# Performance work log

Measured on AMD Instinct MI355X. Metric: run time of the kernel, lower is better.

The kernel has to match this reference:

```python
import jax, jax.numpy as jnp
import numpy as np
from jax import lax

K = 13  # sizearea
DN = ('NCHW', 'OIHW', 'NCHW')


def conv(x, W, b):
    y = lax.conv_general_dilated(x, W, (1, 1), 'SAME', dimension_numbers=DN)
    return y + b[None, :, None, None]


def setup_inputs() -> dict:
    key = jax.random.key(0)
    ks = jax.random.split(key, 4)
    x = jax.random.normal(ks[0], (8, 1, 256, 256), dtype=jnp.float32)
    W1 = jax.random.normal(ks[1], (64, 1, 3, 3), dtype=jnp.float32) * 0.1
    b1 = jnp.zeros((64,), dtype=jnp.float32)
    W2 = jax.random.normal(ks[2], (64, 64, 3, 3), dtype=jnp.float32) * 0.05
    b2 = jnp.zeros((64,), dtype=jnp.float32)
    W3 = jax.random.normal(ks[3], (K * K, 64, 3, 3), dtype=jnp.float32) * 0.05
    b3 = jnp.zeros((K * K,), dtype=jnp.float32)
    return {'x': x, 'W1': W1, 'b1': b1, 'W2': W2, 'b2': b2, 'W3': W3, 'b3': b3}


def reference(x, W1, b1, W2, b2, W3, b3):
    # weight-predicting CNN (sar_data=False -> x used directly)
    h = jax.nn.relu(conv(x, W1, b1))
    h = jax.nn.relu(conv(h, W2, b2))
    w = conv(h, W3, b3)                       # (B, K*K, H, W)

    B, C, H, Wd = x.shape                     # C == 1
    # w.permute(0,2,3,1).view(B,1,H,W,K,K)
    wr = jnp.transpose(w, (0, 2, 3, 1)).reshape(B, 1, H, Wd, K, K)

    Ho, Wo = H - K + 1, Wd - K + 1            # unfold with stride 1, no pad
    pr, pc = (H - Ho) // 2, (Wd - Wo) // 2    # center-crop of weight maps
    wc = wr[:, :, pr:H - pr, pc:Wd - pc]      # (B,1,Ho,Wo,K,K)

    # patches[b,0,i,j,u,v] = x[b,0,i+u,j+v]  (C=1, so channel-major flatten is just (kh,kw))
    patches = lax.conv_general_dilated_patches(
        x, (K, K), (1, 1), 'VALID', dimension_numbers=DN)   # (B, K*K, Ho, Wo)
    patches = patches.reshape(B, 1, K, K, Ho, Wo).transpose(0, 1, 4, 5, 2, 3)

    # per-pixel weighted sum over the KxK window
    y = jnp.einsum('bchwuv,bchwuv->bchw', patches, wc)       # (B,1,Ho,Wo)
    return y
```

## Files before the change

kernel.cpp:

```cpp
#include <hip/hip_runtime.h>

#define HW 256
#define BATCH 8
#define C 64
#define HO 244
#define NPAD 192
#define KTOT 576

typedef __bf16 bf16x8 __attribute__((ext_vector_type(8)));
typedef float f32x16 __attribute__((ext_vector_type(16)));
typedef float f32x2 __attribute__((ext_vector_type(2)));
typedef unsigned short us8 __attribute__((ext_vector_type(8)));

__device__ inline unsigned short fbf(float f) {
    return __builtin_bit_cast(unsigned short, (__bf16)f);
}

__device__ inline float bf2f(unsigned short s) {
    union { unsigned int u; float f; } c;
    c.u = ((unsigned int)s) << 16;
    return c.f;
}

__global__ __launch_bounds__(256) void repack_w_kernel(
    const float* __restrict__ W2, const float* __restrict__ W3,
    unsigned short* __restrict__ B2g, unsigned short* __restrict__ B3g)
{
    int idx = blockIdx.x * 256 + threadIdx.x;
    if (idx < 36 * 2 * C * 8) {
        int e = idx & 7;
        int r = idx >> 3;
        int n = r & 63;
        int s = r >> 6;
        int khalf = s & 1;
        int kstep = s >> 1;
        int chunk = kstep >> 2, ks = kstep & 3;
        int ci = ks * 16 + khalf * 8 + e;
        B2g[idx] = fbf(W2[((size_t)n * C + ci) * 9 + chunk]);
    } else {
        int j = idx - 36 * 2 * C * 8;
        if (j >= 36 * 2 * NPAD * 8) return;
        int e = j & 7;
        int r = j >> 3;
        int n = r % NPAD;
        int s = r / NPAD;
        int khalf = s & 1;
        int kstep = s >> 1;
        int chunk = kstep >> 2, ks = kstep & 3;
        int ci = ks * 16 + khalf * 8 + e;
        float v = (n < 169) ? W3[((size_t)n * C + ci) * 9 + chunk] : 0.f;
        B3g[j] = fbf(v);
    }
}

__global__ __launch_bounds__(256, 3) void conv2_fused_kernel(
    const float* __restrict__ x, const float* __restrict__ W1,
    const float* __restrict__ b1, const unsigned short* __restrict__ W2r,
    const float* __restrict__ b2, unsigned short* __restrict__ h2)
{
    __shared__ unsigned short Ash[396 * 66];
    __shared__ unsigned short Xsh[8 * 68];

    const int t = threadIdx.x;
    const int lane = t & 63;
    const int wave = t >> 6;
    const int b  = blockIdx.z;
    const int h0 = blockIdx.y * 4;
    const int w0 = blockIdx.x * 64;

    const int col   = lane & 31;
    const int khalf = lane >> 5;
    const int mrow_base = wave * 64;

    const float* __restrict__ xplane = x + ((size_t)b << 16);
#pragma unroll
    for (int it = 0; it < 3; ++it) {
        int li = it * 256 + t;
        if (li < 8 * 68) {
            int rr = li / 68, cc = li - rr * 68;
            int hh = h0 - 2 + rr, ww = w0 - 2 + cc;
            bool ok = (hh >= 0) && (hh < HW) && (ww >= 0) && (ww < HW);
            Xsh[li] = ok ? fbf(xplane[hh * HW + ww]) : (unsigned short)0;
        }
    }

    const int g4 = t & 15;
    f32x2 w01[9], w23[9];
    f32x2 bia01, bia23;
    bia01[0] = b1[g4 * 4 + 0]; bia01[1] = b1[g4 * 4 + 1];
    bia23[0] = b1[g4 * 4 + 2]; bia23[1] = b1[g4 * 4 + 3];
#pragma unroll
    for (int q = 0; q < 9; ++q) {
        w01[q][0] = W1[(g4 * 4 + 0) * 9 + q];
        w01[q][1] = W1[(g4 * 4 + 1) * 9 + q];
        w23[q][0] = W1[(g4 * 4 + 2) * 9 + q];
        w23[q][1] = W1[(g4 * 4 + 3) * 9 + q];
    }

    __syncthreads();

    for (int it = 0; it < 25; ++it) {
        int li = it * 256 + t;
        if (li < 6336) {
            int p = li >> 4;
            int pr = p / 66, pc = p - pr * 66;
            int hh = h0 - 1 + pr, ww = w0 - 1 + pc;
            unsigned short ov[4];
            if (hh >= 0 && hh < HW && ww >= 0 && ww < HW) {
                const unsigned short* xb = Xsh + pr * 68 + pc;
                f32x2 a01 = bia01, a23 = bia23;
#pragma unroll
                for (int i = 0; i < 3; ++i)
#pragma unroll
                    for (int j = 0; j < 3; ++j) {
                        float xv = bf2f(xb[i * 68 + j]);
                        f32x2 xv2; xv2[0] = xv; xv2[1] = xv;
                        a01 += xv2 * w01[i * 3 + j];
                        a23 += xv2 * w23[i * 3 + j];
                    }
                ov[0] = fbf(fmaxf(a01[0], 0.f));
                ov[1] = fbf(fmaxf(a01[1], 0.f));
                ov[2] = fbf(fmaxf(a23[0], 0.f));
                ov[3] = fbf(fmaxf(a23[1], 0.f));
            } else {
#pragma unroll
                for (int u = 0; u < 4; ++u) ov[u] = 0;
            }
            *(uint2*)(Ash + p * 66 + g4 * 4) = *(uint2*)ov;
        }
    }

    const unsigned short* bbase = W2r + ((size_t)khalf * C + col) * 8;
    us8 bcur0 = *(const us8*)(bbase);
    us8 bcur1 = *(const us8*)(bbase + 32 * 8);
    us8 bnx0  = *(const us8*)(bbase + (size_t)(2 * C * 8));
    us8 bnx1  = *(const us8*)(bbase + (size_t)(2 * C * 8) + 32 * 8);

    f32x16 acc[2][2];
#pragma unroll
    for (int ai = 0; ai < 2; ++ai)
#pragma unroll
        for (int nb = 0; nb < 2; ++nb)
#pragma unroll
            for (int r = 0; r < 16; ++r) acc[ai][nb][r] = 0.f;

    __syncthreads();

#pragma unroll
    for (int kstep = 0; kstep < 36; ++kstep) {
        const int chunk = kstep >> 2, ks = kstep & 3;
        const int ii = chunk / 3, jj = chunk - ii * 3;
        const int pixbase = (wave + ii) * 66 + jj;
        us8 bn0, bn1;
        if (kstep + 2 < 36) {
            const unsigned short* bp = bbase + (size_t)(kstep + 2) * (2 * C * 8);
            bn0 = *(const us8*)(bp);
            bn1 = *(const us8*)(bp + 32 * 8);
        }
        const int koff = ks * 16 + khalf * 8;
        bf16x8 a0 = __builtin_bit_cast(bf16x8, *(const us8*)(Ash + (pixbase + col) * 66 + koff));
        bf16x8 a1 = __builtin_bit_cast(bf16x8, *(const us8*)(Ash + (pixbase + col + 32) * 66 + koff));
        bf16x8 v0 = __builtin_bit_cast(bf16x8, bcur0);
        bf16x8 v1 = __builtin_bit_cast(bf16x8, bcur1);
        acc[0][0] = __builtin_amdgcn_mfma_f32_32x32x16_bf16(a0, v0, acc[0][0], 0, 0, 0);
        acc[0][1] = __builtin_amdgcn_mfma_f32_32x32x16_bf16(a0, v1, acc[0][1], 0, 0, 0);
        acc[1][0] = __builtin_amdgcn_mfma_f32_32x32x16_bf16(a1, v0, acc[1][0], 0, 0, 0);
        acc[1][1] = __builtin_amdgcn_mfma_f32_32x32x16_bf16(a1, v1, acc[1][1], 0, 0, 0);
        bcur0 = bnx0; bcur1 = bnx1;
        bnx0 = bn0; bnx1 = bn1;
    }

#pragma unroll
    for (int nb = 0; nb < 2; ++nb) {
        const int n = nb * 32 + col;
        const float bias = b2[n];
#pragma unroll
        for (int ai = 0; ai < 2; ++ai) {
#pragma unroll
            for (int r = 0; r < 16; ++r) {
                int m = mrow_base + ai * 32 + (r & 3) + ((r >> 2) << 3) + (khalf << 2);
                int h = h0 + (m >> 6), w = w0 + (m & 63);
                float val = fmaxf(acc[ai][nb][r] + bias, 0.f);
                h2[(((size_t)b * HW + h) * HW + w) * C + n] = fbf(val);
            }
        }
    }
}

__global__ __launch_bounds__(512, 3) void conv3_mfma_kernel(
    const float* __restrict__ x, const unsigned short* __restrict__ h2,
    const unsigned short* __restrict__ Bg, const float* __restrict__ b3,
    float* __restrict__ y)
{
    __shared__ unsigned short Ash[396 * 72];
    __shared__ float Xsh[16 * 77];
    __shared__ float red[8][64];

    const int t = threadIdx.x;
    const int lane = t & 63;
    const int wave = t >> 6;
    const int b   = blockIdx.z;
    const int ho0 = blockIdx.y * 4;
    const int wo0 = blockIdx.x * 64;

    const int col   = lane & 31;
    const int khalf = lane >> 5;
    const int rsel      = wave >> 1;
    const int mrow_base = rsel * 64;
    const int nbase     = (wave & 1) * 96;

    f32x16 acc[2][3];
#pragma unroll
    for (int mi = 0; mi < 2; ++mi)
#pragma unroll
        for (int ni = 0; ni < 3; ++ni)
#pragma unroll
            for (int r = 0; r < 16; ++r) acc[mi][ni][r] = 0.f;

#pragma unroll
    for (int it = 0; it < 7; ++it) {
        int li = it * 512 + t;
        if (li < 396 * 8) {
            int p = li >> 3, g = li & 7;
            int row = p / 66, cl = p - row * 66;
            int ww = wo0 + 5 + cl; ww = ww < 255 ? ww : 255;
            size_t src = (((size_t)b * HW + (ho0 + 5 + row)) * HW + ww) * C + g * 8;
            *(uint4*)(Ash + p * 72 + g * 8) = *(const uint4*)(h2 + src);
        }
    }
    {
        const float* __restrict__ xplane = x + ((size_t)b << 16);
#pragma unroll
        for (int it = 0; it < 3; ++it) {
            int li = it * 512 + t;
            if (li < 16 * 76) {
                int rr = li / 76, cc = li - rr * 76;
                int ww = wo0 + cc; ww = ww < 255 ? ww : 255;
                Xsh[rr * 77 + cc] = xplane[(ho0 + rr) * HW + ww];
            }
        }
    }

    const unsigned short* bbase = Bg + ((size_t)khalf * NPAD + nbase + col) * 8;
    us8 bcur0 = *(const us8*)(bbase);
    us8 bcur1 = *(const us8*)(bbase + 32 * 8);
    us8 bcur2 = *(const us8*)(bbase + 64 * 8);
    us8 bnx0  = *(const us8*)(bbase + (size_t)(2 * NPAD * 8));
    us8 bnx1  = *(const us8*)(bbase + (size_t)(2 * NPAD * 8) + 32 * 8);
    us8 bnx2  = *(const us8*)(bbase + (size_t)(2 * NPAD * 8) + 64 * 8);

    __syncthreads();

#pragma unroll
    for (int kstep = 0; kstep < 36; ++kstep) {
        const int chunk = kstep >> 2, ks = kstep & 3;
        const int ii = chunk / 3, jj = chunk - ii * 3;
        const int pixbase = (rsel + ii) * 66 + jj;
        us8 bn0, bn1, bn2;
        if (kstep + 2 < 36) {
            const unsigned short* bp = bbase + (size_t)(kstep + 2) * (2 * NPAD * 8);
            bn0 = *(const us8*)(bp);
            bn1 = *(const us8*)(bp + 32 * 8);
            bn2 = *(const us8*)(bp + 64 * 8);
        }
        const int koff = ks * 16 + khalf * 8;
        bf16x8 a0 = __builtin_bit_cast(bf16x8, *(const us8*)(Ash + (pixbase + col) * 72 + koff));
        bf16x8 a1 = __builtin_bit_cast(bf16x8, *(const us8*)(Ash + (pixbase + col + 32) * 72 + koff));
        bf16x8 v0 = __builtin_bit_cast(bf16x8, bcur0);
        bf16x8 v1 = __builtin_bit_cast(bf16x8, bcur1);
        bf16x8 v2 = __builtin_bit_cast(bf16x8, bcur2);
        acc[0][0] = __builtin_amdgcn_mfma_f32_32x32x16_bf16(a0, v0, acc[0][0], 0, 0, 0);
        acc[0][1] = __builtin_amdgcn_mfma_f32_32x32x16_bf16(a0, v1, acc[0][1], 0, 0, 0);
        acc[0][2] = __builtin_amdgcn_mfma_f32_32x32x16_bf16(a0, v2, acc[0][2], 0, 0, 0);
        acc[1][0] = __builtin_amdgcn_mfma_f32_32x32x16_bf16(a1, v0, acc[1][0], 0, 0, 0);
        acc[1][1] = __builtin_amdgcn_mfma_f32_32x32x16_bf16(a1, v1, acc[1][1], 0, 0, 0);
        acc[1][2] = __builtin_amdgcn_mfma_f32_32x32x16_bf16(a1, v2, acc[1][2], 0, 0, 0);
        bcur0 = bnx0; bcur1 = bnx1; bcur2 = bnx2;
        bnx0 = bn0; bnx1 = bn1; bnx2 = bn2;
    }

    int   qv[3], uo[3], vo[3];
    float b3v[3];
#pragma unroll
    for (int ni = 0; ni < 3; ++ni) {
        int q = nbase + ni * 32 + col;
        qv[ni] = q;
        int u = q / 13;
        uo[ni] = u;
        vo[ni] = q - u * 13;
        b3v[ni] = (q < 169) ? b3[q] : 0.f;
    }

    float partial[2][16];
#pragma unroll
    for (int mi = 0; mi < 2; ++mi)
#pragma unroll
        for (int r = 0; r < 16; ++r) {
            int mrow = mi * 32 + (r & 3) + ((r >> 2) << 3) + (khalf << 2);
            bool wok = (wo0 + mrow) < HO;
            float p = 0.f;
#pragma unroll
            for (int ni = 0; ni < 3; ++ni) {
                if (qv[ni] < 169 && wok) {
                    float s = acc[mi][ni][r] + b3v[ni];
                    p += s * Xsh[(rsel + uo[ni]) * 77 + mrow + vo[ni]];
                }
            }
            partial[mi][r] = p;
        }

#pragma unroll
    for (int mi = 0; mi < 2; ++mi)
#pragma unroll
        for (int r = 0; r < 16; ++r) {
            float p = partial[mi][r];
#pragma unroll
            for (int d = 1; d < 32; d <<= 1) p += __shfl_xor(p, d, 64);
            partial[mi][r] = p;
        }

    if (col == 0) {
#pragma unroll
        for (int mi = 0; mi < 2; ++mi)
#pragma unroll
            for (int r = 0; r < 16; ++r) {
                int mrow = mi * 32 + (r & 3) + ((r >> 2) << 3) + (khalf << 2);
                red[wave][mrow] = partial[mi][r];
            }
    }
    __syncthreads();

    if (t < 256) {
        int row_sel = t >> 6, m = t & 63;
        float val = red[row_sel * 2][m] + red[row_sel * 2 + 1][m];
        int wo = wo0 + m, ho = ho0 + row_sel;
        if (wo < HO)
            y[((size_t)b * HO + ho) * HO + wo] = val;
    }
}

extern "C" void kernel_launch(void* const* d_in, const int* in_sizes, int n_in,
                              void* d_out, int out_size, void* d_ws, size_t ws_size,
                              hipStream_t stream) {
    const float* x  = (const float*)d_in[0];
    const float* W1 = (const float*)d_in[1];
    const float* b1 = (const float*)d_in[2];
    const float* W2 = (const float*)d_in[3];
    const float* b2 = (const float*)d_in[4];
    const float* W3 = (const float*)d_in[5];
    const float* b3 = (const float*)d_in[6];
    float* out = (float*)d_out;

    unsigned short* h2  = (unsigned short*)d_ws;
    unsigned short* W2r = h2 + (size_t)BATCH * HW * HW * C;
    unsigned short* W3r = W2r + (size_t)36 * 2 * C * 8;

    repack_w_kernel<<<576, 256, 0, stream>>>(W2, W3, W2r, W3r);
    conv2_fused_kernel<<<dim3(4, 64, 8), 256, 0, stream>>>(x, W1, b1, W2r, b2, h2);
    conv3_mfma_kernel<<<dim3(4, 61, 8), 512, 0, stream>>>(x, h2, W3r, b3, out);
}
```

Measured before the change: 240.3 us.

## Register-block conv1 per thread, add MFMA priority, use DPP reductions in epilogue

The first-layer conv in the conv2 kernel now computes six adjacent output pixels per thread from vectorized row loads. This reuses input values across the sliding window and cuts the loop from 25 iterations to 5. The MFMA block in the conv2 k-loop is wrapped in s_setprio to favour matrix issue. The conv3 epilogue loads x values as float4 and replaces the 5-step shfl_xor reduction with DPP row operations. The DPP lane pattern and the choice of col==16 as the writer carry correctness risk, and the larger per-thread accumulator set raises register pressure.

```diff
diff --git a/kernel.cpp b/kernel.cpp
--- a/kernel.cpp
+++ b/kernel.cpp
@@ -9,6 +9,7 @@
 
 typedef __bf16 bf16x8 __attribute__((ext_vector_type(8)));
 typedef float f32x16 __attribute__((ext_vector_type(16)));
+typedef float f32x4 __attribute__((ext_vector_type(4)));
 typedef float f32x2 __attribute__((ext_vector_type(2)));
 typedef unsigned short us8 __attribute__((ext_vector_type(8)));
 
@@ -20,6 +21,13 @@
     union { unsigned int u; float f; } c;
     c.u = ((unsigned int)s) << 16;
     return c.f;
+}
+
+template <int CTRL>
+__device__ inline float dpp_add(float v) {
+    int s = __builtin_bit_cast(int, v);
+    int m = __builtin_amdgcn_update_dpp(s, s, CTRL, 0xF, 0xF, true);
+    return v + __builtin_bit_cast(float, m);
 }
 
 __global__ __launch_bounds__(256) void repack_w_kernel(
@@ -99,34 +107,52 @@
 
     __syncthreads();
 
-    for (int it = 0; it < 25; ++it) {
+#pragma unroll
+    for (int it = 0; it < 5; ++it) {
         int li = it * 256 + t;
-        if (li < 6336) {
-            int p = li >> 4;
-            int pr = p / 66, pc = p - pr * 66;
-            int hh = h0 - 1 + pr, ww = w0 - 1 + pc;
-            unsigned short ov[4];
-            if (hh >= 0 && hh < HW && ww >= 0 && ww < HW) {
-                const unsigned short* xb = Xsh + pr * 68 + pc;
-                f32x2 a01 = bia01, a23 = bia23;
-#pragma unroll
-                for (int i = 0; i < 3; ++i)
+        if (li < 1056) {
+            int w = li >> 4;
+            int pr = w / 11;
+            int pc0 = (w - pr * 11) * 6;
+            int hh = h0 - 1 + pr;
+            bool okrow = (hh >= 0) && (hh < HW);
+            const unsigned short* xb = Xsh + pr * 68 + pc0;
+
+            f32x2 ac01[6], ac23[6];
+#pragma unroll
+            for (int k2 = 0; k2 < 6; ++k2) { ac01[k2] = bia01; ac23[k2] = bia23; }
+
+#pragma unroll
+            for (int i = 0; i < 3; ++i) {
+                us8 xw = *(const us8*)(xb + i * 68);
+                float xr[8];
+#pragma unroll
+                for (int e = 0; e < 8; ++e) xr[e] = bf2f(xw[e]);
+#pragma unroll
+                for (int k2 = 0; k2 < 6; ++k2)
 #pragma unroll
                     for (int j = 0; j < 3; ++j) {
-                        float xv = bf2f(xb[i * 68 + j]);
-                        f32x2 xv2; xv2[0] = xv; xv2[1] = xv;
-                        a01 += xv2 * w01[i * 3 + j];
-                        a23 += xv2 * w23[i * 3 + j];
+                        f32x2 xv2; xv2[0] = xr[k2 + j]; xv2[1] = xr[k2 + j];
+                        ac01[k2] += xv2 * w01[i * 3 + j];
+                        ac23[k2] += xv2 * w23[i * 3 + j];
                     }
-                ov[0] = fbf(fmaxf(a01[0], 0.f));
-                ov[1] = fbf(fmaxf(a01[1], 0.f));
-                ov[2] = fbf(fmaxf(a23[0], 0.f));
-                ov[3] = fbf(fmaxf(a23[1], 0.f));
-            } else {
-#pragma unroll
-                for (int u = 0; u < 4; ++u) ov[u] = 0;
-            }
-            *(uint2*)(Ash + p * 66 + g4 * 4) = *(uint2*)ov;
+            }
+
+#pragma unroll
+            for (int k2 = 0; k2 < 6; ++k2) {
+                int ww = w0 - 1 + pc0 + k2;
+                bool ok = okrow && (ww >= 0) && (ww < HW);
+                unsigned short ov[4];
+                if (ok) {
+                    ov[0] = fbf(fmaxf(ac01[k2][0], 0.f));
+                    ov[1] = fbf(fmaxf(ac01[k2][1], 0.f));
+                    ov[2] = fbf(fmaxf(ac23[k2][0], 0.f));
+                    ov[3] = fbf(fmaxf(ac23[k2][1], 0.f));
+                } else {
+                    ov[0] = 0; ov[1] = 0; ov[2] = 0; ov[3] = 0;
+                }
+                *(uint2*)(Ash + (pr * 66 + pc0 + k2) * 66 + g4 * 4) = *(uint2*)ov;
+            }
         }
     }
 
@@ -162,10 +188,12 @@
         bf16x8 a1 = __builtin_bit_cast(bf16x8, *(const us8*)(Ash + (pixbase + col + 32) * 66 + koff));
         bf16x8 v0 = __builtin_bit_cast(bf16x8, bcur0);
         bf16x8 v1 = __builtin_bit_cast(bf16x8, bcur1);
+        __builtin_amdgcn_s_setprio(1);
         acc[0][0] = __builtin_amdgcn_mfma_f32_32x32x16_bf16(a0, v0, acc[0][0], 0, 0, 0);
         acc[0][1] = __builtin_amdgcn_mfma_f32_32x32x16_bf16(a0, v1, acc[0][1], 0, 0, 0);
         acc[1][0] = __builtin_amdgcn_mfma_f32_32x32x16_bf16(a1, v0, acc[1][0], 0, 0, 0);
         acc[1][1] = __builtin_amdgcn_mfma_f32_32x32x16_bf16(a1, v1, acc[1][1], 0, 0, 0);
+        __builtin_amdgcn_s_setprio(0);
         bcur0 = bnx0; bcur1 = bnx1;
         bnx0 = bn0; bnx1 = bn1;
     }
@@ -206,7 +234,6 @@
     const int col   = lane & 31;
     const int khalf = lane >> 5;
     const int rsel      = wave >> 1;
-    const int mrow_base = rsel * 64;
     const int nbase     = (wave & 1) * 96;
 
     f32x16 acc[2][3];
@@ -291,43 +318,32 @@
         b3v[ni] = (q < 169) ? b3[q] : 0.f;
     }
 
-    float partial[2][16];
 #pragma unroll
     for (int mi = 0; mi < 2; ++mi)
 #pragma unroll
-        for (int r = 0; r < 16; ++r) {
-            int mrow = mi * 32 + (r & 3) + ((r >> 2) << 3) + (khalf << 2);
-            bool wok = (wo0 + mrow) < HO;
-            float p = 0.f;
-#pragma unroll
-            for (int ni = 0; ni < 3; ++ni) {
-                if (qv[ni] < 169 && wok) {
-                    float s = acc[mi][ni][r] + b3v[ni];
-                    p += s * Xsh[(rsel + uo[ni]) * 77 + mrow + vo[ni]];
+        for (int j = 0; j < 4; ++j) {
+            const int m0 = mi * 32 + 8 * j + (khalf << 2);
+            f32x4 xv0 = *(const f32x4*)&Xsh[(rsel + uo[0]) * 77 + m0 + vo[0]];
+            f32x4 xv1 = *(const f32x4*)&Xsh[(rsel + uo[1]) * 77 + m0 + vo[1]];
+            f32x4 xv2 = *(const f32x4*)&Xsh[(rsel + uo[2]) * 77 + m0 + vo[2]];
+#pragma unroll
+            for (int q = 0; q < 4; ++q) {
+                const int r = j * 4 + q;
+                const int mrow = m0 + q;
+                float p = 0.f;
+                if ((wo0 + mrow) < HO) {
+                    if (qv[0] < 169) p += (acc[mi][0][r] + b3v[0]) * xv0[q];
+                    if (qv[1] < 169) p += (acc[mi][1][r] + b3v[1]) * xv1[q];
+                    if (qv[2] < 169) p += (acc[mi][2][r] + b3v[2]) * xv2[q];
                 }
-            }
-            partial[mi][r] = p;
-        }
-
-#pragma unroll
-    for (int mi = 0; mi < 2; ++mi)
-#pragma unroll
-        for (int r = 0; r < 16; ++r) {
-            float p = partial[mi][r];
-#pragma unroll
-            for (int d = 1; d < 32; d <<= 1) p += __shfl_xor(p, d, 64);
-            partial[mi][r] = p;
-        }
-
-    if (col == 0) {
-#pragma unroll
-        for (int mi = 0; mi < 2; ++mi)
-#pragma unroll
-            for (int r = 0; r < 16; ++r) {
-                int mrow = mi * 32 + (r & 3) + ((r >> 2) << 3) + (khalf << 2);
-                red[wave][mrow] = partial[mi][r];
-            }
-    }
+                p = dpp_add<0xB1>(p);
+                p = dpp_add<0x4E>(p);
+                p = dpp_add<0x124>(p);
+                p = dpp_add<0x128>(p);
+                p = dpp_add<0x142>(p);
+                if (col == 16) red[wave][mrow] = p;
+            }
+        }
     __syncthreads();
 
     if (t < 256) {
```

Result: faster. 225.6 us (-6.1%).
